# Optimization experiments

Measured on AMD Instinct MI355X. Metric: run time of the kernel, lower is better.

## Reference

```python
import jax, jax.numpy as jnp
import numpy as np

HSIZE, ESIZE, RSIZE = 256, 32, 64
STEP = 8  # dist=32, step=dist/4
B, A, T = 32, 128, 64

# 16 directional grid-cell bounds, shape [16,1,1] (matches torch constants)
_XMIN = jnp.array([STEP, 0, -STEP, -2 * STEP] * 4, jnp.float32).reshape(16, 1, 1)
_XMAX = jnp.array([2 * STEP, STEP, 0, -STEP] * 4, jnp.float32).reshape(16, 1, 1)
_YMIN = jnp.repeat(jnp.array([-2 * STEP, -STEP, 0, STEP], jnp.float32), 4).reshape(16, 1, 1)
_YMAX = jnp.repeat(jnp.array([-STEP, 0, STEP, 2 * STEP], jnp.float32), 4).reshape(16, 1, 1)


def setup_inputs() -> dict:
    key = jax.random.key(0)
    ks = jax.random.split(key, 20)
    w = lambda k, shape, s=0.05: jax.random.normal(k, shape, jnp.float32) * s
    data = jax.random.uniform(ks[0], (B, A, T, 2), jnp.float32) * 36.0 - 4.0
    return {
        "data": data,
        "tprob": 0,
        "W_r": w(ks[1], (RSIZE, 2)), "b_r": jnp.zeros((RSIZE,), jnp.float32),
        "W_e": w(ks[2], (ESIZE, HSIZE)), "b_e": jnp.zeros((ESIZE,), jnp.float32),
        "W_ih": w(ks[3], (4 * HSIZE, ESIZE * 16 + RSIZE)),
        "W_hh": w(ks[4], (4 * HSIZE, HSIZE)),
        "b_ih": jnp.zeros((4 * HSIZE,), jnp.float32),
        "b_hh": jnp.zeros((4 * HSIZE,), jnp.float32),
        "W_p": w(ks[5], (64, HSIZE + RSIZE)), "b_p": jnp.zeros((64,), jnp.float32),
        "W_p2": w(ks[6], (32, 64)), "b_p2": jnp.zeros((32,), jnp.float32),
        "W_mu": w(ks[7], (2, 32)), "b_mu": jnp.zeros((2,), jnp.float32),
        "W_sd": w(ks[8], (2, 32)), "b_sd": jnp.zeros((2,), jnp.float32),
        "W_cr": w(ks[9], (1, 32)), "b_cr": jnp.zeros((1,), jnp.float32),
    }


def _social(xy, h):
    # xy: [B,A,2] positions, h: [B,A,HSIZE] hidden states
    b, a = xy.shape[0], xy.shape[1]
    diff = xy[:, :, None, :] - xy[:, None, :, :]          # [B,A,A,2], (i,j)=x_i-x_j
    dx = diff[..., 0][:, None, :, :]                       # [B,1,A,A]
    dy = diff[..., 1][:, None, :, :]
    mask = (dx >= _XMIN) & (dx <= _XMAX) & (dy >= _YMIN) & (dy <= _YMAX)  # [B,16,A,A]
    active = xy[:, :, 0] >= 0                              # inactive: x<0
    mask = mask & active[:, None, :, None] & active[:, None, None, :]
    mask = mask & (~jnp.eye(a, dtype=bool))[None, None]    # zero diagonal
    # bmm: aggregate neighbor hiddens per grid cell
    return jnp.einsum('bgij,bjh->bgih', mask.astype(h.dtype), h)  # [B,16,A,HSIZE]


def reference(data, tprob, W_r, b_r, W_e, b_e, W_ih, W_hh, b_ih, b_hh,
              W_p, b_p, W_p2, b_p2, W_mu, b_mu, W_sd, b_sd, W_cr, b_cr):
    # tprob=0 -> teach_prob all zeros (no teacher forcing); dropout in eval mode.
    b, a, t, _ = data.shape
    h0 = jnp.zeros((b * a, HSIZE), data.dtype)
    c0 = jnp.zeros((b * a, HSIZE), data.dtype)

    def step(carry, xt):  # xt: [B,A,2]
        h, c = carry
        r = jax.nn.relu(xt @ W_r.T + b_r)                          # [B,A,64]
        Hs = _social(xt, h.reshape(b, a, HSIZE))                   # [B,16,A,256]
        e = jax.nn.relu(jnp.einsum('bgah,eh->bgae', Hs, W_e) + b_e)  # [B,16,A,32]
        e = e.reshape(b, a, 16 * ESIZE)                            # torch-style reshape
        inp = jnp.concatenate([r, e], -1).reshape(b * a, RSIZE + 16 * ESIZE)
        gates = inp @ W_ih.T + b_ih + h @ W_hh.T + b_hh
        ig, fg, gg, og = jnp.split(gates, 4, axis=-1)              # torch gate order i,f,g,o
        c2 = jax.nn.sigmoid(fg) * c + jax.nn.sigmoid(ig) * jnp.tanh(gg)
        h2 = jax.nn.sigmoid(og) * jnp.tanh(c2)
        inp2 = jnp.concatenate([r, h2.reshape(b, a, HSIZE)], -1)   # [B,A,320]
        out = (inp2 @ W_p.T + b_p) @ W_p2.T + b_p2                 # no activation (as in source)
        mu = out @ W_mu.T + b_mu
        sd = jnp.exp(out @ W_sd.T + b_sd)
        cr = jnp.tanh(out @ W_cr.T + b_cr)
        return (h2, c2), (mu, sd, cr)

    xs = jnp.moveaxis(data, 2, 0)                                  # [T,B,A,2]
    _, (mus, sds, crs) = jax.lax.scan(step, (h0, c0), xs)
    # stack along dim 2 -> [B,A,T,*]
    return (jnp.moveaxis(mus, 0, 2), jnp.moveaxis(sds, 0, 2), jnp.moveaxis(crs, 0, 2))
```

## Files before the change

kernel.cpp:

```cpp
#include <hip/hip_runtime.h>
#include <hip/hip_bf16.h>

#define B_  32
#define A_  128
#define T_  64
#define N_  4096
#define HS  256
#define ES  32
#define RS  64
#define KX  832
#define GD  1024

typedef __attribute__((ext_vector_type(8))) short bf8_t;
typedef __attribute__((ext_vector_type(8))) unsigned short u16x8;
typedef __attribute__((ext_vector_type(4))) float f4_t;
typedef __attribute__((ext_vector_type(2))) float f2_t;

__device__ __forceinline__ unsigned short f2bf(float x) {
  union { float f; unsigned u; } v; v.f = x;
  unsigned u = v.u;
  u += 0x7fffu + ((u >> 16) & 1u);
  return (unsigned short)(u >> 16);
}
__device__ __forceinline__ float bf2f(unsigned short u) {
  union { unsigned u; float f; } v; v.u = ((unsigned)u) << 16; return v.f;
}
__device__ __forceinline__ float sigm(float x) { return 1.f / (1.f + __expf(-x)); }

__device__ __forceinline__ void gload16(const void* g, void* l) {
  __builtin_amdgcn_global_load_lds((const __attribute__((address_space(1))) void*)g,
                                   (__attribute__((address_space(3))) void*)l, 16, 0, 0);
}

__global__ void k_wcat(const float* __restrict__ W_ih, const float* __restrict__ W_hh,
                       const float* __restrict__ b_ih, const float* __restrict__ b_hh,
                       const float* __restrict__ W_e,
                       unsigned short* __restrict__ Wc, float* __restrict__ bsum,
                       unsigned short* __restrict__ Web) {
  int i = blockIdx.x * 256 + threadIdx.x;
  if (i < GD * KX) {
    int mp = i / KX, k = i - mp * KX;
    int nb = mp >> 6, rem = mp & 63, g = rem >> 4, q = rem & 15;
    int mo = g * 256 + nb * 16 + q;
    float v = (k < 576) ? W_ih[mo * 576 + k] : W_hh[mo * 256 + (k - 576)];
    Wc[i] = f2bf(v);
  } else if (i < GD * KX + GD) {
    int j = i - GD * KX;
    int nb = j >> 6, rem = j & 63, g = rem >> 4, q = rem & 15;
    int mo = g * 256 + nb * 16 + q;
    bsum[j] = b_ih[mo] + b_hh[mo];
  } else if (i < GD * KX + GD + ES * HS) {
    int j2 = i - GD * KX - GD;
    Web[j2] = f2bf(W_e[j2]);
  }
}

__global__ __launch_bounds__(320) void k_head(
    const float* __restrict__ W_p, const float* __restrict__ b_p,
    const float* __restrict__ W_p2, const float* __restrict__ b_p2,
    const float* __restrict__ W_mu, const float* __restrict__ b_mu,
    const float* __restrict__ W_sd, const float* __restrict__ b_sd,
    const float* __restrict__ W_cr, const float* __restrict__ b_cr,
    float* __restrict__ Whead, float* __restrict__ bhead) {
  int o = blockIdx.x, tid = threadIdx.x;
  __shared__ float to[64];
  const float* Wo = (o < 2) ? W_mu + o * 32 : (o < 4) ? W_sd + (o - 2) * 32 : W_cr;
  if (tid < 64) {
    float a = 0.f;
    #pragma unroll 8
    for (int c = 0; c < 32; ++c) a += Wo[c] * W_p2[c * 64 + tid];
    to[tid] = a;
  }
  __syncthreads();
  float a = 0.f;
  #pragma unroll 8
  for (int j = 0; j < 64; ++j) a += to[j] * W_p[j * 320 + tid];
  Whead[o * 320 + tid] = a;
  if (tid == 0) {
    float b0 = (o < 2) ? b_mu[o] : (o < 4) ? b_sd[o - 2] : b_cr[0];
    float acc = b0;
    for (int c = 0; c < 32; ++c) acc += Wo[c] * b_p2[c];
    for (int j = 0; j < 64; ++j) acc += to[j] * b_p[j];
    bhead[o] = acc;
  }
}

__device__ __forceinline__ void head_fin_dev(
    const float* __restrict__ data, const float* __restrict__ W_r,
    const float* __restrict__ b_r, const float* __restrict__ Whead,
    const float* __restrict__ bhead, const unsigned short* __restrict__ Xh,
    float* __restrict__ out, int n0, int ts, int tid) {
  int r8 = tid >> 5, ln = tid & 31;
  int n = n0 + r8;
  float s0 = 0.f, s1 = 0.f, s2 = 0.f, s3 = 0.f, s4 = 0.f;
  u16x8 hv = *(const u16x8*)(Xh + (size_t)n * KX + 576 + ln * 8);
  float hf[8];
  #pragma unroll
  for (int k = 0; k < 8; ++k) hf[k] = bf2f(hv[k]);
  #pragma unroll
  for (int k = 0; k < 8; ++k) {
    int kk = 64 + ln * 8 + k;
    s0 += hf[k] * Whead[0 * 320 + kk];
    s1 += hf[k] * Whead[1 * 320 + kk];
    s2 += hf[k] * Whead[2 * 320 + kk];
    s3 += hf[k] * Whead[3 * 320 + kk];
    s4 += hf[k] * Whead[4 * 320 + kk];
  }
  float x0 = data[(n * T_ + ts) * 2 + 0];
  float x1 = data[(n * T_ + ts) * 2 + 1];
  #pragma unroll
  for (int l2 = 0; l2 < 2; ++l2) {
    int l = ln + 32 * l2;
    float rv = fmaxf(x0 * W_r[l * 2] + x1 * W_r[l * 2 + 1] + b_r[l], 0.f);
    s0 += rv * Whead[0 * 320 + l];
    s1 += rv * Whead[1 * 320 + l];
    s2 += rv * Whead[2 * 320 + l];
    s3 += rv * Whead[3 * 320 + l];
    s4 += rv * Whead[4 * 320 + l];
  }
  #pragma unroll
  for (int off = 16; off; off >>= 1) {
    s0 += __shfl_xor(s0, off);
    s1 += __shfl_xor(s1, off);
    s2 += __shfl_xor(s2, off);
    s3 += __shfl_xor(s3, off);
    s4 += __shfl_xor(s4, off);
  }
  if (ln == 0) {
    out[(n * T_ + ts) * 2 + 0] = s0 + bhead[0];
    out[(n * T_ + ts) * 2 + 1] = s1 + bhead[1];
    out[N_ * T_ * 2 + (n * T_ + ts) * 2 + 0] = __expf(s2 + bhead[2]);
    out[N_ * T_ * 2 + (n * T_ + ts) * 2 + 1] = __expf(s3 + bhead[3]);
    out[N_ * T_ * 4 + n * T_ + ts] = tanhf(s4 + bhead[4]);
  }
}

__global__ __launch_bounds__(512) void k_social(
    const float* __restrict__ data, const unsigned short* __restrict__ Web,
    const float* __restrict__ b_e, unsigned short* __restrict__ Xcur,
    const float* __restrict__ Whead, const float* __restrict__ bhead,
    const float* __restrict__ W_r, const float* __restrict__ b_r,
    float* __restrict__ out, int t) {
  int b   = blockIdx.x >> 3;
  int ig8 = blockIdx.x & 7;
  int n0  = b * A_ + ig8 * 16;
  __shared__ float sx[A_], sy[A_];
  __shared__ float shw2[64 * 64];
  __shared__ float smx[16][64][8];
  __shared__ float smy[16][64][8];
  int tid = threadIdx.x;
  if (tid < A_) {
    sx[tid] = data[((b * A_ + tid) * T_ + t) * 2 + 0];
    sy[tid] = data[((b * A_ + tid) * T_ + t) * 2 + 1];
  }
  if (t > 0)
    head_fin_dev(data, W_r, b_r, Whead, bhead, Xcur, out, n0, t - 1, tid);
  for (int u = tid; u < 1024; u += 512) {
    int rr = u >> 6, l = u & 63;
    int n = n0 + rr;
    float x0 = data[(n * T_ + t) * 2 + 0];
    float x1 = data[(n * T_ + t) * 2 + 1];
    Xcur[(size_t)n * KX + l] =
        f2bf(fmaxf(x0 * W_r[l * 2] + x1 * W_r[l * 2 + 1] + b_r[l], 0.f));
  }
  if (t == 0) {
    for (int i = tid; i < 64 * 64; i += 512) shw2[i] = 0.f;
    u16x8 z = (u16x8){0, 0, 0, 0, 0, 0, 0, 0};
    int row = tid >> 5, c8 = tid & 31;
    *(u16x8*)(Xcur + (size_t)(n0 + row) * KX + 576 + c8 * 8) = z;
  } else {
    int w = tid >> 6, lane = tid & 63;
    int lr = lane & 15, lh = lane >> 4;
    const unsigned short* a0p = Xcur + (size_t)(b * A_ + w * 16 + lr) * KX + 576 + lh * 8;
    const unsigned short* b0p = Web + lr * HS + lh * 8;
    const unsigned short* b1p = Web + (16 + lr) * HS + lh * 8;
    f4_t hacc[2];
    hacc[0] = (f4_t){0.f, 0.f, 0.f, 0.f}; hacc[1] = hacc[0];
    #pragma unroll
    for (int kk = 0; kk < 8; ++kk) {
      bf8_t av  = *(const bf8_t*)(a0p + kk * 32);
      bf8_t bv0 = *(const bf8_t*)(b0p + kk * 32);
      bf8_t bv1 = *(const bf8_t*)(b1p + kk * 32);
      hacc[0] = __builtin_amdgcn_mfma_f32_16x16x32_bf16(av, bv0, hacc[0], 0, 0, 0);
      hacc[1] = __builtin_amdgcn_mfma_f32_16x16x32_bf16(av, bv1, hacc[1], 0, 0, 0);
    }
    int ccol = lane & 15, crow4 = (lane >> 4) * 4;
    #pragma unroll
    for (int cb2 = 0; cb2 < 2; ++cb2)
      #pragma unroll
      for (int j = 0; j < 4; ++j) {
        int rr = w * 16 + crow4 + j;
        int c  = cb2 * 16 + ccol;
        shw2[(rr >> 1) * 64 + c * 2 + (rr & 1)] = hacc[cb2][j];
      }
  }
  __syncthreads();

  for (int u = tid; u < 1024; u += 512) {
    int r = u >> 6, jp = u & 63;
    int irow = ig8 * 16 + r;
    float xi = sx[irow], yi = sy[irow];
    bool acti = xi >= 0.f;
    float m0[4], m1[4], nn0[4], nn1[4];
    #pragma unroll
    for (int s = 0; s < 2; ++s) {
      int j = jp * 2 + s;
      float xj = sx[j], yj = sy[j];
      bool v = acti && (xj >= 0.f) && (j != irow);
      float dx = xi - xj, dy = yi - yj;
      float* mm = s ? m1 : m0;
      float* nn = s ? nn1 : nn0;
      mm[0] = (v && dx >= 8.f   && dx <= 16.f) ? 1.f : 0.f;
      mm[1] = (v && dx >= 0.f   && dx <= 8.f ) ? 1.f : 0.f;
      mm[2] = (v && dx >= -8.f  && dx <= 0.f ) ? 1.f : 0.f;
      mm[3] = (v && dx >= -16.f && dx <= -8.f) ? 1.f : 0.f;
      nn[0] = (dy >= -16.f && dy <= -8.f) ? 1.f : 0.f;
      nn[1] = (dy >= -8.f  && dy <= 0.f ) ? 1.f : 0.f;
      nn[2] = (dy >= 0.f   && dy <= 8.f ) ? 1.f : 0.f;
      nn[3] = (dy >= 8.f   && dy <= 16.f) ? 1.f : 0.f;
    }
    float4* px = (float4*)&smx[r][jp][0];
    px[0] = (float4){m0[0], m1[0], m0[1], m1[1]};
    px[1] = (float4){m0[2], m1[2], m0[3], m1[3]};
    float4* py = (float4*)&smy[r][jp][0];
    py[0] = (float4){nn0[0], nn1[0], nn0[1], nn1[1]};
    py[1] = (float4){nn0[2], nn1[2], nn0[3], nn1[3]};
  }
  __syncthreads();

  int half = tid >> 5;
  int lane = tid & 31;
  f2_t acc[16];
  #pragma unroll
  for (int g = 0; g < 16; ++g) acc[g] = (f2_t){0.f, 0.f};
  #pragma unroll 2
  for (int jp = 0; jp < 64; ++jp) {
    f2_t hv = *(const f2_t*)&shw2[jp * 64 + lane * 2];
    float4 xa = ((const float4*)&smx[half][jp][0])[0];
    float4 xb = ((const float4*)&smx[half][jp][0])[1];
    float4 ya = ((const float4*)&smy[half][jp][0])[0];
    float4 yb = ((const float4*)&smy[half][jp][0])[1];
    f2_t mx[4] = {(f2_t){xa.x, xa.y}, (f2_t){xa.z, xa.w},
                  (f2_t){xb.x, xb.y}, (f2_t){xb.z, xb.w}};
    f2_t p[4]  = {(f2_t){ya.x, ya.y} * hv, (f2_t){ya.z, ya.w} * hv,
                  (f2_t){yb.x, yb.y} * hv, (f2_t){yb.z, yb.w} * hv};
    #pragma unroll
    for (int gy = 0; gy < 4; ++gy)
      #pragma unroll
      for (int gx = 0; gx < 4; ++gx)
        acc[gy * 4 + gx] += mx[gx] * p[gy];
  }

  int irow = ig8 * 16 + half;
  float be = b_e[lane];
  int hi = irow >> 4;
  int klo = (irow & 15) * ES + lane;
  #pragma unroll
  for (int g = 0; g < 16; ++g) {
    float e = fmaxf(acc[g][0] + acc[g][1] + be, 0.f);
    int a_out = g * 8 + hi;
    Xcur[(size_t)(b * A_ + a_out) * KX + 64 + klo] = f2bf(e);
  }
}

__global__ __launch_bounds__(512) void k_gemm_lstm(
    const unsigned short* __restrict__ Xcur, const unsigned short* __restrict__ Wc,
    const float* __restrict__ bsum,
    float* __restrict__ cbuf, unsigned short* __restrict__ Xnext, int t) {
  __shared__ unsigned short sA0[128 * 64];
  __shared__ unsigned short sB0[128 * 64];
  __shared__ unsigned short sA1[128 * 64];
  __shared__ unsigned short sB1[128 * 64];

  int bid = blockIdx.x;
  int tm = bid & 31, tc = bid >> 5;
  int row0 = tm * 128, col0 = tc * 128;
  int tid = threadIdx.x;
  int lane = tid & 63;
  int w = tid >> 6;
  int wr = w >> 1, wc = w & 1;
  int lr = lane & 15, lh = lane >> 4;

  int srow = tid >> 3, schunk = tid & 7;
  int gch = (schunk ^ ((srow >> 1) & 7)) * 8;
  const unsigned short* gA = Xcur + (size_t)(row0 + srow) * KX + gch;
  const unsigned short* gB = Wc  + (size_t)(col0 + srow) * KX + gch;

  int aoff[2][2], boff[4][2];
  #pragma unroll
  for (int m = 0; m < 2; ++m)
    #pragma unroll
    for (int kk = 0; kk < 2; ++kk)
      aoff[m][kk] = (wr * 32 + m * 16 + lr) * 64 + ((kk * 4 + lh) ^ ((lr >> 1) & 7)) * 8;
  #pragma unroll
  for (int n = 0; n < 4; ++n)
    #pragma unroll
    for (int kk = 0; kk < 2; ++kk)
      boff[n][kk] = (wc * 64 + n * 16 + lr) * 64 + ((kk * 4 + lh) ^ ((lr >> 1) & 7)) * 8;

  int q = lane & 15;
  float bias_g[4];
  #pragma unroll
  for (int n = 0; n < 4; ++n) bias_g[n] = bsum[col0 + wc * 64 + n * 16 + q];

  f4_t acc[2][4];
  #pragma unroll
  for (int m = 0; m < 2; ++m)
    #pragma unroll
    for (int n = 0; n < 4; ++n) acc[m][n] = (f4_t){0.f, 0.f, 0.f, 0.f};

#define STAGE(pA, pB, kt) do { \
    gload16(gA + (size_t)(kt) * 64, (pA) + tid * 8); \
    gload16(gA + (size_t)64 * KX + (kt) * 64, (pA) + 4096 + tid * 8); \
    gload16(gB + (size_t)(kt) * 64, (pB) + tid * 8); \
    gload16(gB + (size_t)64 * KX + (kt) * 64, (pB) + 4096 + tid * 8); \
  } while (0)

#define COMPUTE(pA, pB) do { \
    _Pragma("unroll") for (int kk = 0; kk < 2; ++kk) { \
      bf8_t a_[2], b_[4]; \
      _Pragma("unroll") for (int m = 0; m < 2; ++m) a_[m] = *(const bf8_t*)((pA) + aoff[m][kk]); \
      _Pragma("unroll") for (int n = 0; n < 4; ++n) b_[n] = *(const bf8_t*)((pB) + boff[n][kk]); \
      _Pragma("unroll") for (int m = 0; m < 2; ++m) \
        _Pragma("unroll") for (int n = 0; n < 4; ++n) \
          acc[m][n] = __builtin_amdgcn_mfma_f32_16x16x32_bf16(a_[m], b_[n], acc[m][n], 0, 0, 0); \
    } \
  } while (0)

  STAGE(sA0, sB0, 0);
  __syncthreads();
  #pragma unroll 1
  for (int kt = 0; kt < 12; kt += 2) {
    STAGE(sA1, sB1, kt + 1);
    COMPUTE(sA0, sB0);
    __syncthreads();
    STAGE(sA0, sB0, kt + 2);
    COMPUTE(sA1, sB1);
    __syncthreads();
  }
  COMPUTE(sA0, sB0);
#undef STAGE
#undef COMPUTE

  int ch = (tc * 2 + wc) * 16 + q;
  int jrow4 = (lane >> 4) * 4;
  #pragma unroll
  for (int m = 0; m < 2; ++m) {
    #pragma unroll
    for (int j = 0; j < 4; ++j) {
      int row = row0 + wr * 32 + m * 16 + jrow4 + j;
      float ig = acc[m][0][j] + bias_g[0];
      float fg = acc[m][1][j] + bias_g[1];
      float gg = acc[m][2][j] + bias_g[2];
      float og = acc[m][3][j] + bias_g[3];
      float cold = (t == 0) ? 0.f : cbuf[(size_t)row * HS + ch];
      float c2 = sigm(fg) * cold + sigm(ig) * tanhf(gg);
      float h2 = sigm(og) * tanhf(c2);
      cbuf[(size_t)row * HS + ch] = c2;
      Xnext[(size_t)row * KX + 576 + ch] = f2bf(h2);
    }
  }
}

__global__ __launch_bounds__(256) void k_fin(
    const float* __restrict__ data, const float* __restrict__ W_r,
    const float* __restrict__ b_r, const float* __restrict__ Whead,
    const float* __restrict__ bhead, const unsigned short* __restrict__ Xh,
    float* __restrict__ out) {
  head_fin_dev(data, W_r, b_r, Whead, bhead, Xh, out,
               blockIdx.x * 8, T_ - 1, threadIdx.x);
}

extern "C" void kernel_launch(void* const* d_in, const int* in_sizes, int n_in,
                              void* d_out, int out_size, void* d_ws, size_t ws_size,
                              hipStream_t stream) {
  const float* data = (const float*)d_in[0];
  const float* W_r  = (const float*)d_in[2];
  const float* b_r  = (const float*)d_in[3];
  const float* W_e  = (const float*)d_in[4];
  const float* b_e  = (const float*)d_in[5];
  const float* W_ih = (const float*)d_in[6];
  const float* W_hh = (const float*)d_in[7];
  const float* b_ih = (const float*)d_in[8];
  const float* b_hh = (const float*)d_in[9];
  const float* W_p  = (const float*)d_in[10];
  const float* b_p  = (const float*)d_in[11];
  const float* W_p2 = (const float*)d_in[12];
  const float* b_p2 = (const float*)d_in[13];
  const float* W_mu = (const float*)d_in[14];
  const float* b_mu = (const float*)d_in[15];
  const float* W_sd = (const float*)d_in[16];
  const float* b_sd = (const float*)d_in[17];
  const float* W_cr = (const float*)d_in[18];
  const float* b_cr = (const float*)d_in[19];
  float* out = (float*)d_out;

  char* ws = (char*)d_ws;
  float* cbuf  = (float*)(ws);
  unsigned short* Xbf0 = (unsigned short*)(ws + (4u  << 20));
  unsigned short* Xbf1 = (unsigned short*)(ws + (11u << 20));
  unsigned short* Wc   = (unsigned short*)(ws + (18u << 20));
  float* bsum  = (float*)(ws + (20u << 20));
  float* Whead = (float*)(ws + (20u << 20) + 8192);
  float* bhead = (float*)(ws + (20u << 20) + 16384);
  unsigned short* Web = (unsigned short*)(ws + (20u << 20) + 20480);

  k_wcat<<<(GD * KX + GD + ES * HS + 255) / 256, 256, 0, stream>>>(
      W_ih, W_hh, b_ih, b_hh, W_e, Wc, bsum, Web);
  k_head<<<5, 320, 0, stream>>>(W_p, b_p, W_p2, b_p2, W_mu, b_mu, W_sd, b_sd, W_cr, b_cr,
                                Whead, bhead);

  for (int t = 0; t < T_; ++t) {
    unsigned short* Xcur  = (t & 1) ? Xbf1 : Xbf0;
    unsigned short* Xnext = (t & 1) ? Xbf0 : Xbf1;
    k_social<<<256, 512, 0, stream>>>(data, Web, b_e, Xcur, Whead, bhead,
                                      W_r, b_r, out, t);
    k_gemm_lstm<<<256, 512, 0, stream>>>(Xcur, Wc, bsum, cbuf, Xnext, t);
  }
  k_fin<<<512, 256, 0, stream>>>(data, W_r, b_r, Whead, bhead, Xbf0, out);
}
```

Baseline: 2.185 ms.

## Deepen LSTM GEMM K-pipeline to four stages with finer k-tiles

The LSTM gate GEMM now uses 32-wide k-tiles instead of 64 and a four-buffer ring that keeps two tiles in flight. Waits use explicit vmcnt and s_barrier instead of __syncthreads after each stage, so global loads can overlap compute longer. The trade-off is twice as many barriers, fewer MFMAs per barrier, and hand-tuned waitcnt logic that relies on gload16 being an async direct-to-LDS load.

```diff
diff --git a/kernel.cpp b/kernel.cpp
--- a/kernel.cpp
+++ b/kernel.cpp
@@ -10,6 +10,7 @@
 #define RS  64
 #define KX  832
 #define GD  1024
+#define NKT 26
 
 typedef __attribute__((ext_vector_type(8))) short bf8_t;
 typedef __attribute__((ext_vector_type(8))) unsigned short u16x8;
@@ -267,10 +268,10 @@
     const unsigned short* __restrict__ Xcur, const unsigned short* __restrict__ Wc,
     const float* __restrict__ bsum,
     float* __restrict__ cbuf, unsigned short* __restrict__ Xnext, int t) {
-  __shared__ unsigned short sA0[128 * 64];
-  __shared__ unsigned short sB0[128 * 64];
-  __shared__ unsigned short sA1[128 * 64];
-  __shared__ unsigned short sB1[128 * 64];
+  __shared__ unsigned short sA0[128 * 32], sB0[128 * 32];
+  __shared__ unsigned short sA1[128 * 32], sB1[128 * 32];
+  __shared__ unsigned short sA2[128 * 32], sB2[128 * 32];
+  __shared__ unsigned short sA3[128 * 32], sB3[128 * 32];
 
   int bid = blockIdx.x;
   int tm = bid & 31, tc = bid >> 5;
@@ -281,67 +282,71 @@
   int wr = w >> 1, wc = w & 1;
   int lr = lane & 15, lh = lane >> 4;
 
-  int srow = tid >> 3, schunk = tid & 7;
-  int gch = (schunk ^ ((srow >> 1) & 7)) * 8;
+  int srow = tid >> 2, schunk = tid & 3;
+  int gch = (schunk ^ ((srow >> 1) & 3)) * 8;
   const unsigned short* gA = Xcur + (size_t)(row0 + srow) * KX + gch;
   const unsigned short* gB = Wc  + (size_t)(col0 + srow) * KX + gch;
 
-  int aoff[2][2], boff[4][2];
+  int swz = (lh ^ ((lr >> 1) & 3)) * 8;
+  int aoff[2], boff[4];
+  #pragma unroll
+  for (int m = 0; m < 2; ++m) aoff[m] = (wr * 32 + m * 16 + lr) * 32 + swz;
+  #pragma unroll
+  for (int n = 0; n < 4; ++n) boff[n] = (wc * 64 + n * 16 + lr) * 32 + swz;
+
+  f4_t acc[2][4];
   #pragma unroll
   for (int m = 0; m < 2; ++m)
     #pragma unroll
-    for (int kk = 0; kk < 2; ++kk)
-      aoff[m][kk] = (wr * 32 + m * 16 + lr) * 64 + ((kk * 4 + lh) ^ ((lr >> 1) & 7)) * 8;
-  #pragma unroll
-  for (int n = 0; n < 4; ++n)
-    #pragma unroll
-    for (int kk = 0; kk < 2; ++kk)
-      boff[n][kk] = (wc * 64 + n * 16 + lr) * 64 + ((kk * 4 + lh) ^ ((lr >> 1) & 7)) * 8;
+    for (int n = 0; n < 4; ++n) acc[m][n] = (f4_t){0.f, 0.f, 0.f, 0.f};
+
+#define STAGE(pA, pB, kt) do { \
+    gload16(gA + (size_t)(kt) * 32, (pA) + tid * 8); \
+    gload16(gB + (size_t)(kt) * 32, (pB) + tid * 8); \
+  } while (0)
+
+#define COMPUTE(pA, pB) do { \
+    bf8_t a_[2], b_[4]; \
+    _Pragma("unroll") for (int m = 0; m < 2; ++m) a_[m] = *(const bf8_t*)((pA) + aoff[m]); \
+    _Pragma("unroll") for (int n = 0; n < 4; ++n) b_[n] = *(const bf8_t*)((pB) + boff[n]); \
+    _Pragma("unroll") for (int m = 0; m < 2; ++m) \
+      _Pragma("unroll") for (int n = 0; n < 4; ++n) \
+        acc[m][n] = __builtin_amdgcn_mfma_f32_16x16x32_bf16(a_[m], b_[n], acc[m][n], 0, 0, 0); \
+  } while (0)
+
+#define ITER(AC, BC, AN, BN, kt) do { \
+    asm volatile("s_waitcnt vmcnt(2)" ::: "memory"); \
+    __builtin_amdgcn_sched_barrier(0); \
+    __builtin_amdgcn_s_barrier(); \
+    STAGE(AN, BN, (kt) + 2); \
+    COMPUTE(AC, BC); \
+  } while (0)
+
+  STAGE(sA0, sB0, 0);
+  STAGE(sA1, sB1, 1);
+  #pragma unroll 1
+  for (int kt = 0; kt < 24; kt += 4) {
+    ITER(sA0, sB0, sA2, sB2, kt);
+    ITER(sA1, sB1, sA3, sB3, kt + 1);
+    ITER(sA2, sB2, sA0, sB0, kt + 2);
+    ITER(sA3, sB3, sA1, sB1, kt + 3);
+  }
+  asm volatile("s_waitcnt vmcnt(2)" ::: "memory");
+  __builtin_amdgcn_sched_barrier(0);
+  __builtin_amdgcn_s_barrier();
+  COMPUTE(sA0, sB0);
+  asm volatile("s_waitcnt vmcnt(0)" ::: "memory");
+  __builtin_amdgcn_sched_barrier(0);
+  __builtin_amdgcn_s_barrier();
+  COMPUTE(sA1, sB1);
+#undef ITER
+#undef STAGE
+#undef COMPUTE
 
   int q = lane & 15;
   float bias_g[4];
   #pragma unroll
   for (int n = 0; n < 4; ++n) bias_g[n] = bsum[col0 + wc * 64 + n * 16 + q];
-
-  f4_t acc[2][4];
-  #pragma unroll
-  for (int m = 0; m < 2; ++m)
-    #pragma unroll
-    for (int n = 0; n < 4; ++n) acc[m][n] = (f4_t){0.f, 0.f, 0.f, 0.f};
-
-#define STAGE(pA, pB, kt) do { \
-    gload16(gA + (size_t)(kt) * 64, (pA) + tid * 8); \
-    gload16(gA + (size_t)64 * KX + (kt) * 64, (pA) + 4096 + tid * 8); \
-    gload16(gB + (size_t)(kt) * 64, (pB) + tid * 8); \
-    gload16(gB + (size_t)64 * KX + (kt) * 64, (pB) + 4096 + tid * 8); \
-  } while (0)
-
-#define COMPUTE(pA, pB) do { \
-    _Pragma("unroll") for (int kk = 0; kk < 2; ++kk) { \
-      bf8_t a_[2], b_[4]; \
-      _Pragma("unroll") for (int m = 0; m < 2; ++m) a_[m] = *(const bf8_t*)((pA) + aoff[m][kk]); \
-      _Pragma("unroll") for (int n = 0; n < 4; ++n) b_[n] = *(const bf8_t*)((pB) + boff[n][kk]); \
-      _Pragma("unroll") for (int m = 0; m < 2; ++m) \
-        _Pragma("unroll") for (int n = 0; n < 4; ++n) \
-          acc[m][n] = __builtin_amdgcn_mfma_f32_16x16x32_bf16(a_[m], b_[n], acc[m][n], 0, 0, 0); \
-    } \
-  } while (0)
-
-  STAGE(sA0, sB0, 0);
-  __syncthreads();
-  #pragma unroll 1
-  for (int kt = 0; kt < 12; kt += 2) {
-    STAGE(sA1, sB1, kt + 1);
-    COMPUTE(sA0, sB0);
-    __syncthreads();
-    STAGE(sA0, sB0, kt + 2);
-    COMPUTE(sA1, sB1);
-    __syncthreads();
-  }
-  COMPUTE(sA0, sB0);
-#undef STAGE
-#undef COMPUTE
-
   int ch = (tc * 2 + wc) * 16 + q;
   int jrow4 = (lane >> 4) * 4;
   #pragma unroll
```

Measured after the change: 2.124 ms. 2.8% less time.
